# Performance work log

Hardware: AMD Instinct MI355X
Metric: run time of the kernel (lower is better)

## Reference

```python
import jax, jax.numpy as jnp
import numpy as np

N, TX, TZ, DX, DZ, DATT, DOUT = 8, 2048, 2048, 1024, 1024, 1024, 1024


def setup_inputs() -> dict:
    key = jax.random.key(0)
    ks = jax.random.split(key, 8)
    s = 0.02
    x = jax.random.normal(ks[0], (N, TX, DX), dtype=jnp.float32)
    z = jax.random.normal(ks[1], (N, TZ, DZ), dtype=jnp.float32)
    Wq = jax.random.normal(ks[2], (DX, DATT), dtype=jnp.float32) * s
    bq = jnp.zeros((DATT,), dtype=jnp.float32)
    Wk = jax.random.normal(ks[3], (DZ, DATT), dtype=jnp.float32) * s
    bk = jnp.zeros((DATT,), dtype=jnp.float32)
    Wv = jax.random.normal(ks[4], (DZ, DOUT), dtype=jnp.float32) * s
    bv = jnp.zeros((DOUT,), dtype=jnp.float32)
    # fixed boolean mask [Tx, Tz]; causal lower-triangular so no row is fully masked
    mask = jnp.tril(jnp.ones((TX, TZ), dtype=bool))
    return {"x": x, "z": z, "Wq": Wq, "bq": bq, "Wk": Wk, "bk": bk,
            "Wv": Wv, "bv": bv, "mask": mask}


def reference(x, z, Wq, bq, Wk, bk, Wv, bv, mask):
    Datt = Wq.shape[1]
    Q = x @ Wq + bq                      # [N, Tx, Datt]
    K = z @ Wk + bk                      # [N, Tz, Datt]
    V = z @ Wv + bv                      # [N, Tz, Dout]
    S = jnp.einsum('bxd,bzd->bxz', Q, K)  # [N, Tx, Tz]
    S = jnp.where(mask[None, :, :], S, -jnp.inf)
    A = jax.nn.softmax(S / jnp.sqrt(jnp.float32(Datt)), axis=-1)
    y = jnp.einsum('bxz,bzo->bxo', A, V)  # [N, Tx, Dout]
    return y
```

## Files before the change

### kernel.cpp

```cpp
#include <hip/hip_runtime.h>

typedef _Float16 f16;
typedef _Float16 f16x8 __attribute__((ext_vector_type(8)));
typedef _Float16 f16x4 __attribute__((ext_vector_type(4)));
typedef float    f32x4 __attribute__((ext_vector_type(4)));

constexpr int NB   = 8;
constexpr int T    = 2048;
constexpr int D    = 1024;
constexpr int SA_BATCH = 36 * 65536;

__device__ __forceinline__ void load_lds16(const f16* g, f16* l) {
    __builtin_amdgcn_global_load_lds(
        (const __attribute__((address_space(1))) void*)g,
        (__attribute__((address_space(3))) void*)l, 16, 0, 0);
}

__global__ __launch_bounds__(256) void cast_transpose_w(
    const float* __restrict__ W0, const float* __restrict__ W1,
    const float* __restrict__ W2, f16* __restrict__ Wt)
{
    __shared__ f16 tile[32][33];
    const int which = blockIdx.z;
    const float* W = which == 0 ? W0 : (which == 1 ? W1 : W2);
    f16* dst = Wt + (size_t)which * D * D;
    const int c0 = blockIdx.x * 32, r0 = blockIdx.y * 32;
    const int tx = threadIdx.x & 31, ty = threadIdx.x >> 5;
    #pragma unroll
    for (int i = 0; i < 32; i += 8)
        tile[ty + i][tx] = (f16)W[(size_t)(r0 + ty + i) * D + c0 + tx];
    __syncthreads();
    #pragma unroll
    for (int i = 0; i < 32; i += 8)
        dst[(size_t)(c0 + ty + i) * D + r0 + tx] = tile[tx][ty + i];
}

__global__ __launch_bounds__(256) void cast_xz(
    const float* __restrict__ x, const float* __restrict__ z,
    f16* __restrict__ xh, f16* __restrict__ zh)
{
    const float* src = blockIdx.y ? z : x;
    f16* dst = blockIdx.y ? zh : xh;
    const size_t i = ((size_t)blockIdx.x * 256 + threadIdx.x) * 4;
    const float4 v = *(const float4*)(src + i);
    f16x4 u = { (f16)v.x, (f16)v.y, (f16)v.z, (f16)v.w };
    *(f16x4*)(dst + i) = u;
}

template<int MODE>
__global__ __launch_bounds__(512, 2) void gemm_nt(
    const f16* __restrict__ Ag_, const f16* __restrict__ Bg_,
    void* __restrict__ Cg_, void* __restrict__ Cg2_,
    const float* __restrict__ bias, const float* __restrict__ bias2,
    float* __restrict__ rsum)
{
    constexpr int BM     = (MODE == 1 || MODE == 2) ? 128 : 256;
    constexpr int MR     = BM / 32;
    constexpr int ALOADS = BM / 64;
    constexpr int SLOADS = ALOADS + 4;

    __shared__ f16 As[2 * BM * 64];
    __shared__ f16 Bs[2 * 256 * 64];

    int bx, by, bz = blockIdx.z;
    if (MODE == 1) {
        const int p = blockIdx.x;
        bz = p & 7;
        const int u = p >> 3;
        int cnt = 1, acc0 = 0; by = 0;
        while (acc0 + cnt <= u) { acc0 += cnt; ++by; cnt = (by >> 1) + 1; }
        bx = u - acc0;
    } else if (MODE == 2) {
        const int xx = blockIdx.x;
        bz = xx & 7; bx = xx >> 3;
        by = 15 - (int)blockIdx.y;
    } else {
        constexpr int GX  = (MODE == 0) ? 4 : 8;
        constexpr int LGX = (MODE == 0) ? 2 : 3;
        constexpr int NWG = GX * 64;
        int id = (int)blockIdx.y * GX + (int)blockIdx.x;
        id = (id & 7) * (NWG >> 3) + (id >> 3);
        bx = id & (GX - 1);
        by = id >> LGX;
    }

    const size_t bm0 = (size_t)by * BM, bn0 = (size_t)bx * 256;
    const f16* Abase; const f16* Bbase;
    int lda, ldb, K;
    if (MODE == 0 || MODE == 4) {
        Abase = Ag_ + bm0 * D;                       lda = D;
        Bbase = Bg_ + bn0 * D;                       ldb = D; K = D;
    } else if (MODE == 1) {
        Abase = Ag_ + (size_t)bz * T * D + bm0 * D;  lda = D;
        Bbase = Bg_ + (size_t)bz * T * D + bn0 * D;  ldb = D; K = D;
    } else {
        const int by2 = by >> 1;
        K = (by2 + 1) * 256; lda = K;
        Abase = Ag_ + (size_t)bz * SA_BATCH + (size_t)(by2 * (by2 + 1) / 2) * 65536
              + (size_t)((by & 1) * 128) * K;
        Bbase = Bg_ + (size_t)bz * D * T + bn0 * T;  ldb = T;
    }

    const int t    = threadIdx.x;
    const int lane = t & 63, wave = t >> 6;
    const int wr   = (wave >> 2) * (BM / 2), wc = (wave & 3) * 64;
    const int fr   = lane & 15, ho = lane >> 4;
    const int srow = t >> 3;
    const int scol = ((t & 7) ^ ((t >> 3) & 7)) * 8;
    const int wub  = wave * 512;
    const f16* Ap = Abase + (size_t)srow * lda + scol;
    const f16* Bp = Bbase + (size_t)srow * ldb + scol;
    const int fsw = fr & 7;

    f32x4 acc[MR][4] = {};
    const int nk = K >> 6;

    auto stage = [&](int s, int b) {
        const size_t k = (size_t)s * 64;
        #pragma unroll
        for (int i = 0; i < ALOADS; ++i)
            load_lds16(Ap + k + (size_t)(i * 64) * lda,
                       As + b * (BM * 64) + i * 4096 + wub);
        #pragma unroll
        for (int i = 0; i < 4; ++i)
            load_lds16(Bp + k + (size_t)(i * 64) * ldb,
                       Bs + b * 16384 + i * 4096 + wub);
    };

    stage(0, 0);

    for (int s = 0; s < nk; ++s) {
        const int cur = s & 1;
        if (s + 1 < nk) {
            stage(s + 1, cur ^ 1);
            if constexpr (SLOADS == 8)
                asm volatile("s_waitcnt vmcnt(8)" ::: "memory");
            else
                asm volatile("s_waitcnt vmcnt(6)" ::: "memory");
        } else {
            asm volatile("s_waitcnt vmcnt(0)" ::: "memory");
        }
        __builtin_amdgcn_sched_barrier(0);
        __builtin_amdgcn_s_barrier();
        __builtin_amdgcn_sched_barrier(0);

        const f16* Ab = As + cur * (BM * 64);
        const f16* Bb = Bs + cur * 16384;
        #pragma unroll
        for (int kc = 0; kc < 2; ++kc) {
            const int ch = (((kc << 2) | ho) ^ fsw) << 3;
            f16x8 av[MR], bv[4];
            #pragma unroll
            for (int i = 0; i < MR; ++i)
                av[i] = *(const f16x8*)&Ab[((wr + i * 16 + fr) << 6) + ch];
            #pragma unroll
            for (int j = 0; j < 4; ++j)
                bv[j] = *(const f16x8*)&Bb[((wc + j * 16 + fr) << 6) + ch];
            __builtin_amdgcn_s_setprio(1);
            #pragma unroll
            for (int i = 0; i < MR; ++i)
                #pragma unroll
                for (int j = 0; j < 4; ++j)
                    acc[i][j] = __builtin_amdgcn_mfma_f32_16x16x32_f16(av[i], bv[j], acc[i][j], 0, 0, 0);
            __builtin_amdgcn_s_setprio(0);
        }
        __builtin_amdgcn_sched_barrier(0);
        __builtin_amdgcn_s_barrier();
    }

    const int cr = (lane >> 4) * 4, cc = lane & 15;
    if (MODE == 0) {
        f16* Cp = (f16*)Cg_;
        #pragma unroll
        for (int j = 0; j < 4; ++j) {
            const int col = (int)bn0 + wc + j * 16 + cc;
            const float bb = bias[col];
            #pragma unroll
            for (int i = 0; i < MR; ++i)
                #pragma unroll
                for (int g = 0; g < 4; ++g)
                    Cp[(bm0 + wr + i * 16 + cr + g) * D + col] = (f16)(acc[i][j][g] + bb);
        }
    } else if (MODE == 4) {
        if (bx < 4) {
            f16* Cp = (f16*)Cg_;
            #pragma unroll
            for (int j = 0; j < 4; ++j) {
                const int col = (int)bn0 + wc + j * 16 + cc;
                const float bb = bias[col];
                #pragma unroll
                for (int i = 0; i < MR; ++i)
                    #pragma unroll
                    for (int g = 0; g < 4; ++g)
                        Cp[(bm0 + wr + i * 16 + cr + g) * D + col] = (f16)(acc[i][j][g] + bb);
            }
        } else {
            f16* Vt = (f16*)Cg2_;
            const int b  = (int)(bm0 >> 11);
            const int r0 = (int)(bm0 & 2047);
            #pragma unroll
            for (int j = 0; j < 4; ++j) {
                const int colv = (int)bn0 - 1024 + wc + j * 16 + cc;
                const float bb = bias2[colv];
                #pragma unroll
                for (int i = 0; i < MR; ++i) {
                    f16x4 pk = { (f16)(acc[i][j][0] + bb), (f16)(acc[i][j][1] + bb),
                                 (f16)(acc[i][j][2] + bb), (f16)(acc[i][j][3] + bb) };
                    *(f16x4*)&Vt[(size_t)b * D * T + (size_t)colv * T + r0 + wr + i * 16 + cr] = pk;
                }
            }
        }
    } else if (MODE == 1) {
        const int by2  = by >> 1;
        const int ldab = (by2 + 1) * 256;
        f16* Cp = (f16*)Cg_ + (size_t)bz * SA_BATCH
                + (size_t)(by2 * (by2 + 1) / 2) * 65536
                + (size_t)((by & 1) * 128) * ldab + bn0;
        float* rs = rsum + (size_t)bz * T + bm0;
        #pragma unroll
        for (int i = 0; i < MR; ++i) {
            float rowsum[4] = {};
            #pragma unroll
            for (int j = 0; j < 4; ++j)
                #pragma unroll
                for (int g = 0; g < 4; ++g) {
                    const int lr = wr + i * 16 + cr + g, lc = wc + j * 16 + cc;
                    const int r = (int)bm0 + lr, c = (int)bn0 + lc;
                    const float p = (c > r) ? 0.0f : __expf(acc[i][j][g] * 0.03125f);
                    Cp[(size_t)lr * ldab + lc] = (f16)p;
                    rowsum[g] += p;
                }
            #pragma unroll
            for (int g = 0; g < 4; ++g) {
                float sv = rowsum[g];
                sv += __shfl_xor(sv, 1, 64);
                sv += __shfl_xor(sv, 2, 64);
                sv += __shfl_xor(sv, 4, 64);
                sv += __shfl_xor(sv, 8, 64);
                if (cc == 0) atomicAdd(&rs[wr + i * 16 + cr + g], sv);
            }
        }
    } else {
        float* Cp = (float*)Cg_ + (size_t)bz * T * D;
        const float* rs = rsum + (size_t)bz * T;
        #pragma unroll
        for (int i = 0; i < MR; ++i) {
            const int r4 = (int)bm0 + wr + i * 16 + cr;
            float rinv[4];
            #pragma unroll
            for (int g = 0; g < 4; ++g) rinv[g] = 1.0f / rs[r4 + g];
            #pragma unroll
            for (int j = 0; j < 4; ++j)
                #pragma unroll
                for (int g = 0; g < 4; ++g)
                    Cp[(size_t)(r4 + g) * D + bn0 + wc + j * 16 + cc] = acc[i][j][g] * rinv[g];
        }
    }
}

extern "C" void kernel_launch(void* const* d_in, const int* in_sizes, int n_in,
                              void* d_out, int out_size, void* d_ws, size_t ws_size,
                              hipStream_t stream)
{
    const float* x  = (const float*)d_in[0];
    const float* z  = (const float*)d_in[1];
    const float* Wq = (const float*)d_in[2];
    const float* bq = (const float*)d_in[3];
    const float* Wk = (const float*)d_in[4];
    const float* bk = (const float*)d_in[5];
    const float* Wv = (const float*)d_in[6];
    const float* bv = (const float*)d_in[7];
    float* out = (float*)d_out;

    char* ws = (char*)d_ws;
    f16*   Wt   = (f16*)(ws);
    f16*   xh   = (f16*)(ws + 6291456ull);
    f16*   zh   = (f16*)(ws + 39845888ull);
    f16*   Qh   = (f16*)(ws + 73400320ull);
    f16*   Kh   = (f16*)(ws + 106954752ull);
    f16*   Vt   = (f16*)(ws + 140509184ull);
    f16*   SA   = (f16*)(ws + 6291456ull);
    float* rsum = (float*)(ws + 209715200ull);

    hipMemsetAsync(rsum, 0, (size_t)NB * T * sizeof(float), stream);
    cast_transpose_w<<<dim3(32, 32, 3), 256, 0, stream>>>(Wq, Wk, Wv, Wt);
    cast_xz<<<dim3(16384, 2, 1), 256, 0, stream>>>(x, z, xh, zh);
    gemm_nt<0><<<dim3(4, 64, 1), 512, 0, stream>>>(xh, Wt, Qh, nullptr, bq, nullptr, nullptr);
    gemm_nt<4><<<dim3(8, 64, 1), 512, 0, stream>>>(zh, Wt + 1048576, Kh, Vt, bk, bv, nullptr);
    gemm_nt<1><<<dim3(576, 1, 1), 512, 0, stream>>>(Qh, Kh, SA, nullptr, nullptr, nullptr, rsum);
    gemm_nt<2><<<dim3(32, 16, 1), 512, 0, stream>>>(SA, Vt, out, nullptr, nullptr, nullptr, rsum);
}
```

Before: 442.8 us.

## Split GEMM K-tiles into half-stages with interleaved loads and MFMA phases

Restructures the gemm_nt main loop so each 64-wide K tile is split into two 32-wide halves held in a four-slot LDS ring. Global-to-LDS loads for the next halves are issued between four MFMA sub-phases, with finer vmcnt waits and barriers. The aim is to overlap memory traffic with compute more evenly and keep the LDS reads for one sub-phase ahead of its MFMAs. The cost is more barriers per tile, and the new swizzle and wait counts must exactly match the load issue order.

```diff
diff --git a/kernel.cpp b/kernel.cpp
--- a/kernel.cpp
+++ b/kernel.cpp
@@ -15,6 +15,10 @@
         (const __attribute__((address_space(1))) void*)g,
         (__attribute__((address_space(3))) void*)l, 16, 0, 0);
 }
+
+#define WAITV(N) asm volatile("s_waitcnt vmcnt(" #N ")" ::: "memory")
+#define BAR2()  do { __builtin_amdgcn_s_barrier(); \
+                     __builtin_amdgcn_sched_barrier(0); } while (0)
 
 __global__ __launch_bounds__(256) void cast_transpose_w(
     const float* __restrict__ W0, const float* __restrict__ W1,
@@ -54,13 +58,13 @@
     const float* __restrict__ bias, const float* __restrict__ bias2,
     float* __restrict__ rsum)
 {
-    constexpr int BM     = (MODE == 1 || MODE == 2) ? 128 : 256;
-    constexpr int MR     = BM / 32;
-    constexpr int ALOADS = BM / 64;
-    constexpr int SLOADS = ALOADS + 4;
-
-    __shared__ f16 As[2 * BM * 64];
-    __shared__ f16 Bs[2 * 256 * 64];
+    constexpr int BM  = (MODE == 1 || MODE == 2) ? 128 : 256;
+    constexpr int MR  = BM / 32;
+    constexpr int MR2 = MR / 2;
+    constexpr int AI  = BM / 128;
+
+    __shared__ f16 Al[4 * BM * 32];
+    __shared__ f16 Bl[4 * 256 * 32];
 
     int bx, by, bz = blockIdx.z;
     if (MODE == 1) {
@@ -104,68 +108,112 @@
     const int t    = threadIdx.x;
     const int lane = t & 63, wave = t >> 6;
     const int wr   = (wave >> 2) * (BM / 2), wc = (wave & 3) * 64;
-    const int fr   = lane & 15, ho = lane >> 4;
-    const int srow = t >> 3;
-    const int scol = ((t & 7) ^ ((t >> 3) & 7)) * 8;
+    const int fr   = lane & 15;
+    const int csw  = (((lane >> 4) ^ ((lane >> 1) & 3)) << 3);
+    const int sr   = t >> 2;
+    const int sc   = (((t & 3) ^ ((t >> 3) & 3)) << 3);
     const int wub  = wave * 512;
-    const f16* Ap = Abase + (size_t)srow * lda + scol;
-    const f16* Bp = Bbase + (size_t)srow * ldb + scol;
-    const int fsw = fr & 7;
+    const f16* ApS = Abase + (size_t)sr * lda + sc;
+    const f16* BpS = Bbase + (size_t)sr * ldb + sc;
 
     f32x4 acc[MR][4] = {};
     const int nk = K >> 6;
 
-    auto stage = [&](int s, int b) {
-        const size_t k = (size_t)s * 64;
-        #pragma unroll
-        for (int i = 0; i < ALOADS; ++i)
-            load_lds16(Ap + k + (size_t)(i * 64) * lda,
-                       As + b * (BM * 64) + i * 4096 + wub);
-        #pragma unroll
-        for (int i = 0; i < 4; ++i)
-            load_lds16(Bp + k + (size_t)(i * 64) * ldb,
-                       Bs + b * 16384 + i * 4096 + wub);
+    auto stageA = [&](int kt, int h, int db) {
+        const size_t k = (size_t)kt * 64 + h * 32;
+        #pragma unroll
+        for (int j = 0; j < AI; ++j)
+            load_lds16(ApS + k + (size_t)(j * 128) * lda,
+                       Al + ((db * 2 + h) * BM + j * 128) * 32 + wub);
     };
-
-    stage(0, 0);
-
-    for (int s = 0; s < nk; ++s) {
-        const int cur = s & 1;
-        if (s + 1 < nk) {
-            stage(s + 1, cur ^ 1);
-            if constexpr (SLOADS == 8)
-                asm volatile("s_waitcnt vmcnt(8)" ::: "memory");
-            else
-                asm volatile("s_waitcnt vmcnt(6)" ::: "memory");
-        } else {
-            asm volatile("s_waitcnt vmcnt(0)" ::: "memory");
-        }
-        __builtin_amdgcn_sched_barrier(0);
-        __builtin_amdgcn_s_barrier();
-        __builtin_amdgcn_sched_barrier(0);
-
-        const f16* Ab = As + cur * (BM * 64);
-        const f16* Bb = Bs + cur * 16384;
-        #pragma unroll
-        for (int kc = 0; kc < 2; ++kc) {
-            const int ch = (((kc << 2) | ho) ^ fsw) << 3;
-            f16x8 av[MR], bv[4];
-            #pragma unroll
-            for (int i = 0; i < MR; ++i)
-                av[i] = *(const f16x8*)&Ab[((wr + i * 16 + fr) << 6) + ch];
-            #pragma unroll
-            for (int j = 0; j < 4; ++j)
-                bv[j] = *(const f16x8*)&Bb[((wc + j * 16 + fr) << 6) + ch];
-            __builtin_amdgcn_s_setprio(1);
-            #pragma unroll
-            for (int i = 0; i < MR; ++i)
-                #pragma unroll
-                for (int j = 0; j < 4; ++j)
-                    acc[i][j] = __builtin_amdgcn_mfma_f32_16x16x32_f16(av[i], bv[j], acc[i][j], 0, 0, 0);
-            __builtin_amdgcn_s_setprio(0);
-        }
-        __builtin_amdgcn_sched_barrier(0);
-        __builtin_amdgcn_s_barrier();
+    auto stageB = [&](int kt, int h, int db) {
+        const size_t k = (size_t)kt * 64 + h * 32;
+        #pragma unroll
+        for (int j = 0; j < 2; ++j)
+            load_lds16(BpS + k + (size_t)(j * 128) * ldb,
+                       Bl + ((db * 2 + h) * 256 + j * 128) * 32 + wub);
+    };
+
+    stageA(0, 0, 0); stageB(0, 0, 0);
+    stageA(0, 1, 0); stageB(0, 1, 0);
+    if (1 < nk) { stageA(1, 0, 1); stageB(1, 0, 1); }
+    if constexpr (BM == 256) WAITV(8); else WAITV(6);
+    BAR2();
+
+    for (int tk = 0; tk < nk; ++tk) {
+        const int db = tk & 1, dn = db ^ 1;
+        const f16* A0 = Al + (db * 2 + 0) * BM * 32;
+        const f16* A1 = Al + (db * 2 + 1) * BM * 32;
+        const f16* B0 = Bl + (db * 2 + 0) * 256 * 32;
+        const f16* B1 = Bl + (db * 2 + 1) * 256 * 32;
+        f16x8 av[MR2], bv[4];
+
+        #pragma unroll
+        for (int i = 0; i < MR2; ++i)
+            av[i] = *(const f16x8*)&A0[(wr + i * 16 + fr) * 32 + csw];
+        #pragma unroll
+        for (int j = 0; j < 4; ++j)
+            bv[j] = *(const f16x8*)&B0[(wc + j * 16 + fr) * 32 + csw];
+        if (tk + 1 < nk) stageA(tk + 1, 1, dn);
+        BAR2();
+        __builtin_amdgcn_s_setprio(1);
+        #pragma unroll
+        for (int i = 0; i < MR2; ++i)
+            #pragma unroll
+            for (int j = 0; j < 4; ++j)
+                acc[i][j] = __builtin_amdgcn_mfma_f32_16x16x32_f16(av[i], bv[j], acc[i][j], 0, 0, 0);
+        __builtin_amdgcn_s_setprio(0);
+        BAR2();
+
+        #pragma unroll
+        for (int i = 0; i < MR2; ++i)
+            av[i] = *(const f16x8*)&A0[(wr + (MR2 + i) * 16 + fr) * 32 + csw];
+        if (tk + 1 < nk) stageB(tk + 1, 1, dn);
+        if (tk + 1 < nk) { if constexpr (BM == 256) WAITV(8); else WAITV(6); }
+        else WAITV(0);
+        BAR2();
+        __builtin_amdgcn_s_setprio(1);
+        #pragma unroll
+        for (int i = 0; i < MR2; ++i)
+            #pragma unroll
+            for (int j = 0; j < 4; ++j)
+                acc[MR2 + i][j] = __builtin_amdgcn_mfma_f32_16x16x32_f16(av[i], bv[j], acc[MR2 + i][j], 0, 0, 0);
+        __builtin_amdgcn_s_setprio(0);
+        BAR2();
+
+        #pragma unroll
+        for (int i = 0; i < MR2; ++i)
+            av[i] = *(const f16x8*)&A1[(wr + i * 16 + fr) * 32 + csw];
+        #pragma unroll
+        for (int j = 0; j < 4; ++j)
+            bv[j] = *(const f16x8*)&B1[(wc + j * 16 + fr) * 32 + csw];
+        if (tk + 2 < nk) stageA(tk + 2, 0, db);
+        BAR2();
+        __builtin_amdgcn_s_setprio(1);
+        #pragma unroll
+        for (int i = 0; i < MR2; ++i)
+            #pragma unroll
+            for (int j = 0; j < 4; ++j)
+                acc[i][j] = __builtin_amdgcn_mfma_f32_16x16x32_f16(av[i], bv[j], acc[i][j], 0, 0, 0);
+        __builtin_amdgcn_s_setprio(0);
+        BAR2();
+
+        #pragma unroll
+        for (int i = 0; i < MR2; ++i)
+            av[i] = *(const f16x8*)&A1[(wr + (MR2 + i) * 16 + fr) * 32 + csw];
+        if (tk + 2 < nk) stageB(tk + 2, 0, db);
+        if (tk + 2 < nk)      { if constexpr (BM == 256) WAITV(8); else WAITV(6); }
+        else if (tk + 1 < nk) { if constexpr (BM == 256) WAITV(4); else WAITV(3); }
+        else WAITV(0);
+        BAR2();
+        __builtin_amdgcn_s_setprio(1);
+        #pragma unroll
+        for (int i = 0; i < MR2; ++i)
+            #pragma unroll
+            for (int j = 0; j < 4; ++j)
+                acc[MR2 + i][j] = __builtin_amdgcn_mfma_f32_16x16x32_f16(av[i], bv[j], acc[MR2 + i][j], 0, 0, 0);
+        __builtin_amdgcn_s_setprio(0);
+        BAR2();
     }
 
     const int cr = (lane >> 4) * 4, cc = lane & 15;
```

After: 468.2 us. 5.7% more time.
